# Kernel tuning notes

Hardware: AMD Instinct MI355X
Metric: run time of the kernel (lower is better)

The kernel has to match this reference:

```python
import jax, jax.numpy as jnp
import numpy as np

G = 16          # grid_size
U = 4           # num_controls
C = 4           # num_classes
B = 2048        # batch_size
HID = 64        # SegNet hidden channels (SegNet source unavailable; simple conv encoder assumed)
L = 1.0e6       # 'infinite' cost, matches C++ init g = 1e6
K = G * G       # value-iteration sweeps: upper bound on optimal path hop count
MOVES = [(-1, 0), (1, 0), (0, -1), (0, 1)]  # 4-connected controls


def conv2d(x, w, b):
    # x: (B,Cin,H,W), w: (Cout,Cin,3,3) SAME padding
    y = jax.lax.conv_general_dilated(x, w, (1, 1), 'SAME',
                                     dimension_numbers=('NCHW', 'OIHW', 'NCHW'))
    return y + b[None, :, None, None]


def neighbors(g):
    # g: (B,G,G) cost-to-go; returns (B,U,G,G) = g at x+move_u, L outside grid
    p = jnp.pad(g, ((0, 0), (1, 1), (1, 1)), constant_values=L)
    return jnp.stack([p[:, 1 + dr:1 + dr + G, 1 + dc:1 + dc + G] for dr, dc in MOVES], axis=1)


def shortest_path_Q(cost, loc, goal):
    # cost: (B,U,G,G) positive c(x,u); exact grid shortest-path via Bellman value iteration,
    # equivalent to the batched A* of the C++ extension.
    b_idx = jnp.arange(B)
    g0 = jnp.full((B, G, G), L, dtype=cost.dtype)
    g0 = g0.at[b_idx, goal[:, 0], goal[:, 1]].set(0.0)

    def step(g, _):
        g_new = jnp.minimum(g, jnp.min(cost + neighbors(g), axis=1))
        return g_new, None

    g, _ = jax.lax.scan(step, g0, None, length=K)
    Qmap = cost + neighbors(g)                       # (B,U,G,G): Q(x,u)
    # gather Q(start, u); loc in [1,G-1) so x+move stays on-grid
    return Qmap[b_idx[:, None], jnp.arange(U)[None, :], loc[:, 0:1], loc[:, 1:2]]


def setup_inputs() -> dict:
    key = jax.random.key(0)
    ks = jax.random.split(key, 6)
    grid_cnt = jax.random.uniform(ks[0], (B, C, G, G), dtype=jnp.float32) * 10.0
    loc = jax.random.randint(ks[1], (B, 2), 1, G - 1)
    goal = jax.random.randint(ks[2], (B, 2), 1, G - 1)
    theta = jnp.ones((C, G, G), dtype=jnp.float32)
    w1 = jax.random.normal(ks[3], (HID, C, 3, 3), dtype=jnp.float32) * 0.1
    b1 = jnp.zeros((HID,), dtype=jnp.float32)
    w2 = jax.random.normal(ks[4], (U, HID, 3, 3), dtype=jnp.float32) * 0.1
    b2 = jnp.zeros((U,), dtype=jnp.float32)
    return {"grid_cnt_batch": grid_cnt, "loc_batch": loc, "goal_batch": goal,
            "theta": theta, "w1": w1, "b1": b1, "w2": w2, "b2": b2}


def reference(grid_cnt_batch, loc_batch, goal_batch, theta, w1, b1, w2, b2):
    # map_encoder: per-pixel softmax over classes of grid_cnt * theta
    sem_prob = jax.nn.softmax(grid_cnt_batch * theta[None], axis=1)   # (B,C,G,G)
    # cost_encoder (SegNet stand-in): conv-relu-conv-softplus, strictly positive costs
    h = jax.nn.relu(conv2d(sem_prob, w1, b1))                          # (B,HID,G,G)
    cost = jax.nn.softplus(conv2d(h, w2, b2)) + 1e-6                   # (B,U,G,G)
    Q = shortest_path_Q(cost, loc_batch, goal_batch)                   # (B,U)
    logit = -Q
    return logit, jax.nn.softmax(logit, axis=1)
```

## Files before the change

### kernel.cpp

```cpp
#include <hip/hip_runtime.h>
#include <math.h>

#define GSZ   16
#define NPIX  256
#define LBIG  1.0e6f
#define PW    18
#define PP18  324
#define HBS   (PP18 * 16)

typedef __fp16 f16x8 __attribute__((ext_vector_type(8)));
typedef float  f32x4 __attribute__((ext_vector_type(4)));
typedef __fp16 h2v   __attribute__((ext_vector_type(2)));
union UH2 { unsigned u; h2v h; };
union F8U { f16x8 h; uint4 u; unsigned w[4]; };
union UF  { unsigned u; float f; };

__device__ __forceinline__ unsigned pk2(float a, float b) {
    UH2 u; u.h = __builtin_amdgcn_cvt_pkrtz(a, b);
    return u.u;
}
__device__ __forceinline__ float dpp_up1(float x) {
    UF s; s.f = x;
    UF r; r.u = __builtin_amdgcn_update_dpp(0, (int)s.u, 0x111, 0xF, 0xF, true);
    return r.f;
}
__device__ __forceinline__ float dpp_dn1(float x) {
    UF s; s.f = x;
    UF r; r.u = __builtin_amdgcn_update_dpp(0, (int)s.u, 0x101, 0xF, 0xF, true);
    return r.f;
}

__global__ void pack_weights(const float* __restrict__ w1,
                             const float* __restrict__ w2,
                             __fp16* __restrict__ pw) {
    int i = blockIdx.x * 256 + threadIdx.x;
    if (i < 4096) {
        int j = i & 7, lane = (i >> 3) & 63, t = i >> 9;
        int ks = t >> 2, nt = t & 3;
        int oc = nt * 16 + (lane & 15);
        int k  = ks * 32 + ((lane >> 4) & 3) * 8 + j;
        int tap = k >> 2, cls = k & 3;
        pw[i] = (tap < 9) ? (__fp16)w1[oc * 36 + cls * 9 + tap] : (__fp16)0.0f;
    } else if (i < 4096 + 9216) {
        int m = i - 4096;
        int j = m & 7, lane = (m >> 3) & 63, t = m >> 9;
        int ks = t & 1, tap = t >> 1;
        int u  = lane & 15;
        int oc = ks * 32 + ((lane >> 4) & 3) * 8 + j;
        pw[i] = (u < 4) ? (__fp16)w2[u * 576 + oc * 9 + tap] : (__fp16)0.0f;
    }
}

__device__ __forceinline__ int ring_idx(int t) {
    return (t < 18) ? t
         : (t < 36) ? (306 + (t - 18))
         : (t < 52) ? ((t - 35) * PW)
                    : ((t - 51) * PW + 17);
}

__global__ __launch_bounds__(256, 2) void semirl_kernel(
    const float*  __restrict__ grid_cnt,
    const int*    __restrict__ loc,
    const int*    __restrict__ goal,
    const float*  __restrict__ theta,
    const float*  __restrict__ b1,
    const float*  __restrict__ b2,
    const __fp16* __restrict__ pw,
    float*        __restrict__ out,
    int B)
{
    const int b0   = blockIdx.x * 4;
    const int tid  = threadIdx.x;
    const int lane = tid & 63;
    const int wv   = tid >> 6;
    const int g    = (lane >> 4) & 3;
    const int ln   = lane & 15;

    __shared__ uint2 s_sem[PP18];
    __shared__ uint4 s_h4[8 * PP18];
    __shared__ float s_cost[4][4][NPIX];
    __shared__ float s_gout[4][NPIX];
    char* s_hb = (char*)s_h4;

    F8U w1f[2][4];
    {
        const uint4* p1 = (const uint4*)pw;
        #pragma unroll
        for (int ks = 0; ks < 2; ++ks)
            #pragma unroll
            for (int nt = 0; nt < 4; ++nt)
                w1f[ks][nt].u = p1[(ks * 4 + nt) * 64 + lane];
    }
    F8U w2f[9][2];
    {
        const uint4* p2 = (const uint4*)(pw + 4096);
        #pragma unroll
        for (int tp = 0; tp < 9; ++tp)
            #pragma unroll
            for (int ks = 0; ks < 2; ++ks)
                w2f[tp][ks].u = p2[(tp * 2 + ks) * 64 + lane];
    }
    float4 bias1v[4];
    #pragma unroll
    for (int nt = 0; nt < 4; ++nt)
        bias1v[nt] = *(const float4*)&b1[nt * 16 + g * 4];
    const float4 b2v = *(const float4*)b2;

    const int eidx = b0 + wv;
    const int grr = goal[2 * eidx], gcc = goal[2 * eidx + 1];
    const int lr  = loc[2 * eidx],  lc  = loc[2 * eidx + 1];

    float th[4], gi[4][4];
    #pragma unroll
    for (int c = 0; c < 4; ++c) th[c] = theta[c * NPIX + tid];
    #pragma unroll
    for (int e = 0; e < 4; ++e)
        #pragma unroll
        for (int c = 0; c < 4; ++c)
            gi[e][c] = grid_cnt[(size_t)(b0 + e) * (4 * NPIX) + c * NPIX + tid];

    if (tid < 68) s_sem[ring_idx(tid)] = make_uint2(0u, 0u);
    for (int i2 = tid; i2 < 544; i2 += 256) {
        int qq = ring_idx(i2 >> 3);
        s_h4[(i2 & 7) * PP18 + qq] = make_uint4(0u, 0u, 0u, 0u);
    }
    const int pr = tid >> 4, pc = tid & 15;
    {
        float x0 = gi[0][0] * th[0], x1 = gi[0][1] * th[1];
        float x2 = gi[0][2] * th[2], x3 = gi[0][3] * th[3];
        float m  = fmaxf(fmaxf(x0, x1), fmaxf(x2, x3));
        float e0 = __expf(x0 - m), e1 = __expf(x1 - m);
        float e2 = __expf(x2 - m), e3 = __expf(x3 - m);
        float inv = 1.0f / (e0 + e1 + e2 + e3);
        s_sem[(pr + 1) * PW + (pc + 1)] =
            make_uint2(pk2(e0 * inv, e1 * inv), pk2(e2 * inv, e3 * inv));
    }
    __syncthreads();

    const int off0 = (g == 0) ? (-PW - 1) : (g == 1) ? (-PW + 1) : (g == 2) ? 0 : (PW - 1);
    const int off1 = (g == 0) ? (-PW)     : (g == 1) ? (-1)      : (g == 2) ? 1 : PW;
    const int OFF[9] = { -PW - 1, -PW, -PW + 1, -1, 0, 1, PW - 1, PW, PW + 1 };

    #pragma unroll
    for (int e = 0; e < 4; ++e) {
        #pragma unroll
        for (int i = 0; i < 4; ++i) {
            const int mt = wv * 4 + i;
            const int pp = (mt + 1) * PW + (ln + 1);
            const uint2 A0 = s_sem[pp + off0];
            const uint2 A1 = s_sem[pp + off1];
            const uint2 A2 = s_sem[pp + (PW + 1)];
            F8U a0, a1;
            a0.w[0] = A0.x; a0.w[1] = A0.y; a0.w[2] = A1.x; a0.w[3] = A1.y;
            a1.w[0] = A2.x; a1.w[1] = A2.y; a1.w[2] = 0u;  a1.w[3] = 0u;
            char* wbase = s_hb + (g >> 1) * HBS + pp * 16 + (g & 1) * 8;
            #pragma unroll
            for (int nt = 0; nt < 4; ++nt) {
                f32x4 acc = { bias1v[nt].x, bias1v[nt].y, bias1v[nt].z, bias1v[nt].w };
                acc = __builtin_amdgcn_mfma_f32_16x16x32_f16(w1f[0][nt].h, a0.h, acc, 0, 0, 0);
                acc = __builtin_amdgcn_mfma_f32_16x16x32_f16(w1f[1][nt].h, a1.h, acc, 0, 0, 0);
                uint2 hv;
                hv.x = pk2(fmaxf(acc[0], 0.0f), fmaxf(acc[1], 0.0f));
                hv.y = pk2(fmaxf(acc[2], 0.0f), fmaxf(acc[3], 0.0f));
                *(uint2*)(wbase + nt * (2 * HBS)) = hv;
            }
        }
        __syncthreads();

        #pragma unroll
        for (int i = 0; i < 4; ++i) {
            const int mt = wv * 4 + i;
            const int pp = (mt + 1) * PW + (ln + 1);
            const char* hb0 = s_hb + g * HBS + pp * 16;
            const char* hb1 = hb0 + 4 * HBS;
            f32x4 cacc;
            cacc[0] = (g == 0) ? b2v.x : 0.0f;
            cacc[1] = (g == 0) ? b2v.y : 0.0f;
            cacc[2] = (g == 0) ? b2v.z : 0.0f;
            cacc[3] = (g == 0) ? b2v.w : 0.0f;
            #pragma unroll
            for (int tp = 0; tp < 9; ++tp) {
                F8U af;
                af.u = *(const uint4*)(hb0 + OFF[tp] * 16);
                cacc = __builtin_amdgcn_mfma_f32_16x16x32_f16(w2f[tp][0].h, af.h, cacc, 0, 0, 0);
                af.u = *(const uint4*)(hb1 + OFF[tp] * 16);
                cacc = __builtin_amdgcn_mfma_f32_16x16x32_f16(w2f[tp][1].h, af.h, cacc, 0, 0, 0);
            }
            if (g == 0) {
                #pragma unroll
                for (int reg = 0; reg < 4; ++reg) {
                    float x = cacc[reg];
                    s_cost[e][reg][mt * 16 + ln] =
                        fmaxf(x, 0.0f) + __logf(1.0f + __expf(-fabsf(x))) + 1e-6f;
                }
            }
        }
        if (e < 3) {
            float x0 = gi[e+1][0] * th[0], x1 = gi[e+1][1] * th[1];
            float x2 = gi[e+1][2] * th[2], x3 = gi[e+1][3] * th[3];
            float m  = fmaxf(fmaxf(x0, x1), fmaxf(x2, x3));
            float e0 = __expf(x0 - m), e1 = __expf(x1 - m);
            float e2 = __expf(x2 - m), e3 = __expf(x3 - m);
            float inv = 1.0f / (e0 + e1 + e2 + e3);
            s_sem[(pr + 1) * PW + (pc + 1)] =
                make_uint2(pk2(e0 * inv, e1 * inv), pk2(e2 * inv, e3 * inv));
        }
        __syncthreads();
    }

    {
        const int cv  = ln;
        const int rgv = g;
        const int r0  = rgv * 4;

        float cs[4][4];
        #pragma unroll
        for (int i = 0; i < 4; ++i)
            #pragma unroll
            for (int u = 0; u < 4; ++u)
                cs[i][u] = s_cost[wv][u][(r0 + i) * GSZ + cv];

        float gg[4];
        #pragma unroll
        for (int i = 0; i < 4; ++i)
            gg[i] = (cv == gcc && (r0 + i) == grr) ? 0.0f : LBIG;

        for (int k = 0; k < 128; ++k) {
            const float gu = __shfl_up(gg[3], 16);
            const float gd = __shfl_down(gg[0], 16);
            const float up0 = (rgv > 0) ? gu : LBIG;
            const float dn3 = (rgv < 3) ? gd : LBIG;
            bool ch = false;
            #pragma unroll
            for (int s = 0; s < 2; ++s) {
                float lf[4], rt[4];
                #pragma unroll
                for (int i = 0; i < 4; ++i) { lf[i] = dpp_up1(gg[i]); rt[i] = dpp_dn1(gg[i]); }
                #pragma unroll
                for (int i = 0; i < 4; ++i) {
                    lf[i] = (cv > 0)  ? lf[i] : LBIG;
                    rt[i] = (cv < 15) ? rt[i] : LBIG;
                }
                const float up[4] = { up0, gg[0], gg[1], gg[2] };
                const float dn[4] = { gg[1], gg[2], gg[3], dn3 };
                #pragma unroll
                for (int i = 0; i < 4; ++i) {
                    float q = fminf(fminf(cs[i][0] + up[i], cs[i][1] + dn[i]),
                                    fminf(cs[i][2] + lf[i], cs[i][3] + rt[i]));
                    float ng = fminf(gg[i], q);
                    ch = ch || (ng < gg[i]);
                    gg[i] = ng;
                }
            }
            if (__ballot(ch) == 0ULL) break;
        }

        #pragma unroll
        for (int i = 0; i < 4; ++i)
            s_gout[wv][(r0 + i) * GSZ + cv] = gg[i];
    }

    if (lane == 0) {
        const int lp = lr * GSZ + lc;
        float Q0 = s_cost[wv][0][lp] + s_gout[wv][lp - GSZ];
        float Q1 = s_cost[wv][1][lp] + s_gout[wv][lp + GSZ];
        float Q2 = s_cost[wv][2][lp] + s_gout[wv][lp - 1];
        float Q3 = s_cost[wv][3][lp] + s_gout[wv][lp + 1];
        float l0 = -Q0, l1 = -Q1, l2 = -Q2, l3 = -Q3;
        float m  = fmaxf(fmaxf(l0, l1), fmaxf(l2, l3));
        float e0 = __expf(l0 - m), e1 = __expf(l1 - m);
        float e2 = __expf(l2 - m), e3 = __expf(l3 - m);
        float inv = 1.0f / (e0 + e1 + e2 + e3);
        float* lo = out + (size_t)eidx * 4;
        float* po = out + (size_t)B * 4 + (size_t)eidx * 4;
        lo[0] = l0; lo[1] = l1; lo[2] = l2; lo[3] = l3;
        po[0] = e0 * inv; po[1] = e1 * inv; po[2] = e2 * inv; po[3] = e3 * inv;
    }
}

extern "C" void kernel_launch(void* const* d_in, const int* in_sizes, int n_in,
                              void* d_out, int out_size, void* d_ws, size_t ws_size,
                              hipStream_t stream) {
    const float* grid_cnt = (const float*)d_in[0];
    const int*   loc      = (const int*)  d_in[1];
    const int*   goal     = (const int*)  d_in[2];
    const float* theta    = (const float*)d_in[3];
    const float* w1       = (const float*)d_in[4];
    const float* b1       = (const float*)d_in[5];
    const float* w2       = (const float*)d_in[6];
    const float* b2       = (const float*)d_in[7];
    float*       outp     = (float*)d_out;
    __fp16*      pw       = (__fp16*)d_ws;
    const int B = in_sizes[1] / 2;

    hipLaunchKernelGGL(pack_weights, dim3(52), dim3(256), 0, stream, w1, w2, pw);
    hipLaunchKernelGGL(semirl_kernel, dim3(B / 4), dim3(256), 0, stream,
                       grid_cnt, loc, goal, theta, b1, b2, pw, outp, B);
}
```

Measured before the change: 33.77 us.

## Process two elements per block with fp16 cost storage to raise occupancy

Each 256-thread block now handles two batch elements instead of four, which doubles the grid size and raises the launch-bounds occupancy target from 2 to 3 blocks per CU. Costs are stored as packed fp16 in shared memory, and the value-iteration output reuses the hidden-activation buffer, shrinking LDS per block. Only two of the four waves run the Bellman iteration, so half the waves sit idle in that phase. The fp16 cost rounding may introduce small numerical differences.

```diff
diff --git a/kernel.cpp b/kernel.cpp
--- a/kernel.cpp
+++ b/kernel.cpp
@@ -58,7 +58,7 @@
                     : ((t - 51) * PW + 17);
 }
 
-__global__ __launch_bounds__(256, 2) void semirl_kernel(
+__global__ __launch_bounds__(256, 3) void semirl_kernel(
     const float*  __restrict__ grid_cnt,
     const int*    __restrict__ loc,
     const int*    __restrict__ goal,
@@ -69,7 +69,7 @@
     float*        __restrict__ out,
     int B)
 {
-    const int b0   = blockIdx.x * 4;
+    const int b0   = blockIdx.x * 2;
     const int tid  = threadIdx.x;
     const int lane = tid & 63;
     const int wv   = tid >> 6;
@@ -78,9 +78,9 @@
 
     __shared__ uint2 s_sem[PP18];
     __shared__ uint4 s_h4[8 * PP18];
-    __shared__ float s_cost[4][4][NPIX];
-    __shared__ float s_gout[4][NPIX];
-    char* s_hb = (char*)s_h4;
+    __shared__ uint2 s_costh[2][NPIX];
+    char*  s_hb   = (char*)s_h4;
+    float* s_gout = (float*)s_h4;
 
     F8U w1f[2][4];
     {
@@ -106,15 +106,15 @@
         bias1v[nt] = *(const float4*)&b1[nt * 16 + g * 4];
     const float4 b2v = *(const float4*)b2;
 
-    const int eidx = b0 + wv;
+    const int eidx = b0 + (wv & 1);
     const int grr = goal[2 * eidx], gcc = goal[2 * eidx + 1];
     const int lr  = loc[2 * eidx],  lc  = loc[2 * eidx + 1];
 
-    float th[4], gi[4][4];
+    float th[4], gi[2][4];
     #pragma unroll
     for (int c = 0; c < 4; ++c) th[c] = theta[c * NPIX + tid];
     #pragma unroll
-    for (int e = 0; e < 4; ++e)
+    for (int e = 0; e < 2; ++e)
         #pragma unroll
         for (int c = 0; c < 4; ++c)
             gi[e][c] = grid_cnt[(size_t)(b0 + e) * (4 * NPIX) + c * NPIX + tid];
@@ -142,7 +142,7 @@
     const int OFF[9] = { -PW - 1, -PW, -PW + 1, -1, 0, 1, PW - 1, PW, PW + 1 };
 
     #pragma unroll
-    for (int e = 0; e < 4; ++e) {
+    for (int e = 0; e < 2; ++e) {
         #pragma unroll
         for (int i = 0; i < 4; ++i) {
             const int mt = wv * 4 + i;
@@ -187,17 +187,17 @@
                 cacc = __builtin_amdgcn_mfma_f32_16x16x32_f16(w2f[tp][1].h, af.h, cacc, 0, 0, 0);
             }
             if (g == 0) {
-                #pragma unroll
-                for (int reg = 0; reg < 4; ++reg) {
-                    float x = cacc[reg];
-                    s_cost[e][reg][mt * 16 + ln] =
-                        fmaxf(x, 0.0f) + __logf(1.0f + __expf(-fabsf(x))) + 1e-6f;
-                }
+                float c0, c1, c2, c3;
+                c0 = fmaxf(cacc[0], 0.0f) + __logf(1.0f + __expf(-fabsf(cacc[0]))) + 1e-6f;
+                c1 = fmaxf(cacc[1], 0.0f) + __logf(1.0f + __expf(-fabsf(cacc[1]))) + 1e-6f;
+                c2 = fmaxf(cacc[2], 0.0f) + __logf(1.0f + __expf(-fabsf(cacc[2]))) + 1e-6f;
+                c3 = fmaxf(cacc[3], 0.0f) + __logf(1.0f + __expf(-fabsf(cacc[3]))) + 1e-6f;
+                s_costh[e][mt * 16 + ln] = make_uint2(pk2(c0, c1), pk2(c2, c3));
             }
         }
-        if (e < 3) {
-            float x0 = gi[e+1][0] * th[0], x1 = gi[e+1][1] * th[1];
-            float x2 = gi[e+1][2] * th[2], x3 = gi[e+1][3] * th[3];
+        if (e < 1) {
+            float x0 = gi[1][0] * th[0], x1 = gi[1][1] * th[1];
+            float x2 = gi[1][2] * th[2], x3 = gi[1][3] * th[3];
             float m  = fmaxf(fmaxf(x0, x1), fmaxf(x2, x3));
             float e0 = __expf(x0 - m), e1 = __expf(x1 - m);
             float e2 = __expf(x2 - m), e3 = __expf(x3 - m);
@@ -208,17 +208,19 @@
         __syncthreads();
     }
 
-    {
+    if (wv < 2) {
         const int cv  = ln;
         const int rgv = g;
         const int r0  = rgv * 4;
 
         float cs[4][4];
         #pragma unroll
-        for (int i = 0; i < 4; ++i)
-            #pragma unroll
-            for (int u = 0; u < 4; ++u)
-                cs[i][u] = s_cost[wv][u][(r0 + i) * GSZ + cv];
+        for (int i = 0; i < 4; ++i) {
+            const uint2 cw = s_costh[wv][(r0 + i) * GSZ + cv];
+            UH2 a, bq; a.u = cw.x; bq.u = cw.y;
+            cs[i][0] = (float)a.h[0];  cs[i][1] = (float)a.h[1];
+            cs[i][2] = (float)bq.h[0]; cs[i][3] = (float)bq.h[1];
+        }
 
         float gg[4];
         #pragma unroll
@@ -257,24 +259,26 @@
 
         #pragma unroll
         for (int i = 0; i < 4; ++i)
-            s_gout[wv][(r0 + i) * GSZ + cv] = gg[i];
-    }
-
-    if (lane == 0) {
-        const int lp = lr * GSZ + lc;
-        float Q0 = s_cost[wv][0][lp] + s_gout[wv][lp - GSZ];
-        float Q1 = s_cost[wv][1][lp] + s_gout[wv][lp + GSZ];
-        float Q2 = s_cost[wv][2][lp] + s_gout[wv][lp - 1];
-        float Q3 = s_cost[wv][3][lp] + s_gout[wv][lp + 1];
-        float l0 = -Q0, l1 = -Q1, l2 = -Q2, l3 = -Q3;
-        float m  = fmaxf(fmaxf(l0, l1), fmaxf(l2, l3));
-        float e0 = __expf(l0 - m), e1 = __expf(l1 - m);
-        float e2 = __expf(l2 - m), e3 = __expf(l3 - m);
-        float inv = 1.0f / (e0 + e1 + e2 + e3);
-        float* lo = out + (size_t)eidx * 4;
-        float* po = out + (size_t)B * 4 + (size_t)eidx * 4;
-        lo[0] = l0; lo[1] = l1; lo[2] = l2; lo[3] = l3;
-        po[0] = e0 * inv; po[1] = e1 * inv; po[2] = e2 * inv; po[3] = e3 * inv;
+            s_gout[wv * NPIX + (r0 + i) * GSZ + cv] = gg[i];
+
+        if (lane == 0) {
+            const int lp = lr * GSZ + lc;
+            const uint2 cw = s_costh[wv][lp];
+            UH2 a, bq; a.u = cw.x; bq.u = cw.y;
+            float Q0 = (float)a.h[0]  + s_gout[wv * NPIX + lp - GSZ];
+            float Q1 = (float)a.h[1]  + s_gout[wv * NPIX + lp + GSZ];
+            float Q2 = (float)bq.h[0] + s_gout[wv * NPIX + lp - 1];
+            float Q3 = (float)bq.h[1] + s_gout[wv * NPIX + lp + 1];
+            float l0 = -Q0, l1 = -Q1, l2 = -Q2, l3 = -Q3;
+            float m  = fmaxf(fmaxf(l0, l1), fmaxf(l2, l3));
+            float e0 = __expf(l0 - m), e1 = __expf(l1 - m);
+            float e2 = __expf(l2 - m), e3 = __expf(l3 - m);
+            float inv = 1.0f / (e0 + e1 + e2 + e3);
+            float* lo = out + (size_t)eidx * 4;
+            float* po = out + (size_t)B * 4 + (size_t)eidx * 4;
+            lo[0] = l0; lo[1] = l1; lo[2] = l2; lo[3] = l3;
+            po[0] = e0 * inv; po[1] = e1 * inv; po[2] = e2 * inv; po[3] = e3 * inv;
+        }
     }
 }
 
@@ -294,6 +298,6 @@
     const int B = in_sizes[1] / 2;
 
     hipLaunchKernelGGL(pack_weights, dim3(52), dim3(256), 0, stream, w1, w2, pw);
-    hipLaunchKernelGGL(semirl_kernel, dim3(B / 4), dim3(256), 0, stream,
+    hipLaunchKernelGGL(semirl_kernel, dim3(B / 2), dim3(256), 0, stream,
                        grid_cnt, loc, goal, theta, b1, b2, pw, outp, B);
 }
```

Measured after the change: 44.63 us. +32.2%, slower.
